# Kernel tuning notes

Hardware: AMD Instinct MI355X
Metric: run time of the kernel (lower is better)

## Reference

```python
import jax, jax.numpy as jnp
import numpy as np

B, N, QD = 2, 4096, 512
HEADS, DIM_HEAD = 8, 64
INNER = HEADS * DIM_HEAD  # 512
SCALE = DIM_HEAD ** -0.5


def setup_inputs() -> dict:
    key = jax.random.key(0)
    ks = jax.random.split(key, 6)
    s = 0.02
    return {
        "x": jax.random.normal(ks[0], (B, N, QD), dtype=jnp.float32),
        "Wq": jax.random.normal(ks[1], (QD, INNER), dtype=jnp.float32) * s,
        "Wk": jax.random.normal(ks[2], (QD, INNER), dtype=jnp.float32) * s,
        "Wv": jax.random.normal(ks[3], (QD, INNER), dtype=jnp.float32) * s,
        "Wo": jax.random.normal(ks[4], (INNER, QD), dtype=jnp.float32) * s,
        "bo": jnp.zeros((QD,), dtype=jnp.float32),
    }


def reference(x, Wq, Wk, Wv, Wo, bo):
    # self-attention: context = x; mask = None; attention_sf = False
    q = x @ Wq  # [B, N, INNER]
    k = x @ Wk
    v = x @ Wv
    # split heads: [B, H, N, D]
    def split(t):
        return t.reshape(B, N, HEADS, DIM_HEAD).transpose(0, 2, 1, 3)
    q, k, v = split(q), split(k), split(v)
    # fp32 QK^T (ATTN_PRECISION='fp32' path)
    sim = jnp.einsum('bhid,bhjd->bhij', q.astype(jnp.float32), k.astype(jnp.float32)) * SCALE
    attn = jax.nn.softmax(sim, axis=-1)
    out = jnp.einsum('bhij,bhjd->bhid', attn, v)  # [B, H, N, D]
    out = out.transpose(0, 2, 1, 3).reshape(B, N, INNER)
    return out @ Wo + bo  # Dropout(p=0) is identity
```

## Files before the change

### kernel.cpp

```cpp
#include <hip/hip_runtime.h>
#include <hip/hip_bf16.h>


typedef __attribute__((ext_vector_type(8))) short short8;
typedef __attribute__((ext_vector_type(4))) float floatx4;
typedef __attribute__((ext_vector_type(16))) float floatx16;

#define MFMA16(a, b, c) __builtin_amdgcn_mfma_f32_16x16x32_bf16((a), (b), (c), 0, 0, 0)
#define MFMA32(a, b, c) __builtin_amdgcn_mfma_f32_32x32x16_bf16((a), (b), (c), 0, 0, 0)

#if __has_builtin(__builtin_amdgcn_exp2f)
#define EXP2(x) __builtin_amdgcn_exp2f(x)
#else
#define EXP2(x) exp2f(x)
#endif

#define QSCALE 0.18033688011112042f

static __device__ __forceinline__ unsigned short f2b(float f) {
  unsigned int u = __float_as_uint(f);
  u += 0x7FFFu + ((u >> 16) & 1u);
  return (unsigned short)(u >> 16);
}

static __device__ __forceinline__ unsigned int pkb(float a, float b) {
  float2 t{a, b};
  __hip_bfloat162 h = __float22bfloat162_rn(t);
  union { __hip_bfloat162 h2; unsigned int u; } cv;
  cv.h2 = h;
  return cv.u;
}

static __device__ __forceinline__ void dma16(const unsigned short* g,
                                             unsigned short* l) {
  __builtin_amdgcn_global_load_lds(
      (const __attribute__((address_space(1))) unsigned int*)g,
      (__attribute__((address_space(3))) unsigned int*)l, 16, 0, 0);
}

__global__ __launch_bounds__(256) void prep_kernel(
    const float* __restrict__ Wq, const float* __restrict__ Wk,
    const float* __restrict__ Wv, const float* __restrict__ Wo,
    const float* __restrict__ x, unsigned short* __restrict__ wtq,
    unsigned short* __restrict__ wtk, unsigned short* __restrict__ wtv,
    unsigned short* __restrict__ wto, unsigned short* __restrict__ xb) {
  const int z = blockIdx.z;
  const int tid = threadIdx.x;
  if (z >= 4) {
    const int bid = (z - 4) * 256 + blockIdx.y * 16 + blockIdx.x;
    const int idx = (bid * 256 + tid) * 8;
    const float4 a = *(const float4*)(x + idx);
    const float4 b = *(const float4*)(x + idx + 4);
    unsigned int u[4] = {pkb(a.x, a.y), pkb(a.z, a.w), pkb(b.x, b.y),
                         pkb(b.z, b.w)};
    *(short8*)(xb + idx) = *(short8*)u;
    return;
  }
  const float* __restrict__ W = (z == 0) ? Wq : (z == 1) ? Wk : (z == 2) ? Wv : Wo;
  unsigned short* __restrict__ T = (z == 0) ? wtq : (z == 1) ? wtk : (z == 2) ? wtv : wto;
  const int k0 = blockIdx.x * 32, c0 = blockIdx.y * 32;
  __shared__ float Ts[32][33];
  const int r = tid >> 3, cc = (tid & 7) * 4;
  const float4 v = *(const float4*)(W + (k0 + r) * 512 + c0 + cc);
  Ts[r][cc] = v.x; Ts[r][cc + 1] = v.y; Ts[r][cc + 2] = v.z; Ts[r][cc + 3] = v.w;
  __syncthreads();
  const unsigned long long uu =
      (unsigned long long)pkb(Ts[cc][r], Ts[cc + 1][r]) |
      ((unsigned long long)pkb(Ts[cc + 2][r], Ts[cc + 3][r]) << 32);
  *(unsigned long long*)(T + (c0 + r) * 512 + k0 + cc) = uu;
}

__global__ __launch_bounds__(256) void qkv_fused_kernel(
    const unsigned short* __restrict__ xb, const unsigned short* __restrict__ wtq,
    const unsigned short* __restrict__ wtk,
    const unsigned short* __restrict__ wtv, unsigned short* __restrict__ qo,
    unsigned short* __restrict__ ko, unsigned short* __restrict__ vo) {
  const int m0 = blockIdx.x * 128;
  const int c0 = blockIdx.y * 32;
  __shared__ __align__(16) unsigned short As[2][128 * 64];
  __shared__ __align__(16) unsigned short Bs[2][3][32 * 64];
  const int tid = threadIdx.x;
  const int lane = tid & 63, w = tid >> 6;
  const int i = lane & 15, q = lane >> 4;
  const int sl = i & 7;
  const int dr = lane >> 3, dc = lane & 7;
  const int sch = (dc ^ dr) * 8;
  const unsigned short* ag = xb + (m0 + w * 32 + dr) * 512 + sch;
  const unsigned short* bg[3];
  bg[0] = wtq + (c0 + w * 8 + dr) * 512 + sch;
  bg[1] = wtk + (c0 + w * 8 + dr) * 512 + sch;
  bg[2] = wtv + (c0 + w * 8 + dr) * 512 + sch;

  floatx4 acc[3][2][2] = {};

#pragma unroll
  for (int p = 0; p < 4; ++p) dma16(ag + p * 8 * 512, &As[0][(w * 32 + p * 8) * 64]);
#pragma unroll
  for (int z = 0; z < 3; ++z) dma16(bg[z], &Bs[0][z][(w * 8) * 64]);
  __syncthreads();

  int buf = 0;
  for (int ks = 0; ks < 8; ++ks) {
    if (ks < 7) {
      const int k1 = (ks + 1) * 64;
#pragma unroll
      for (int p = 0; p < 4; ++p)
        dma16(ag + p * 8 * 512 + k1, &As[buf ^ 1][(w * 32 + p * 8) * 64]);
#pragma unroll
      for (int z = 0; z < 3; ++z)
        dma16(bg[z] + k1, &Bs[buf ^ 1][z][(w * 8) * 64]);
    }
#pragma unroll
    for (int kc = 0; kc < 2; ++kc) {
      short8 af[2];
#pragma unroll
      for (int t = 0; t < 2; ++t)
        af[t] = *(const short8*)&As[buf][(w * 32 + t * 16 + i) * 64 +
                                        (((kc * 4 + q) ^ sl) * 8)];
#pragma unroll
      for (int z = 0; z < 3; ++z)
#pragma unroll
        for (int g = 0; g < 2; ++g) {
          const short8 bf = *(const short8*)&Bs[buf][z][(g * 16 + i) * 64 +
                                                        (((kc * 4 + q) ^ sl) * 8)];
#pragma unroll
          for (int t = 0; t < 2; ++t)
            acc[z][t][g] = MFMA16(af[t], bf, acc[z][t][g]);
        }
    }
    __syncthreads();
    buf ^= 1;
  }
#pragma unroll
  for (int z = 0; z < 3; ++z)
#pragma unroll
    for (int t = 0; t < 2; ++t)
#pragma unroll
      for (int g = 0; g < 2; ++g) {
        const int col = c0 + g * 16 + i;
        const int h = col >> 6, d = col & 63;
        const int row0 = m0 + w * 32 + t * 16 + q * 4;
        const int b = row0 >> 12;
        const int n0 = row0 & 4095;
        if (z == 2) {
          unsigned int* dst =
              (unsigned int*)&vo[(((b * 8 + h) * 64 + d) << 12) + n0];
          dst[0] = pkb(acc[z][t][g][0], acc[z][t][g][1]);
          dst[1] = pkb(acc[z][t][g][2], acc[z][t][g][3]);
        } else {
          unsigned short* dst = (z == 0) ? qo : ko;
          const float sc = (z == 0) ? QSCALE : 1.0f;
#pragma unroll
          for (int r = 0; r < 4; ++r)
            dst[(((b * 8 + h) << 12) + (n0 + r)) * 64 + d] =
                f2b(acc[z][t][g][r] * sc);
        }
      }
}

__global__ __launch_bounds__(512, 4) void flash_kernel(
    const unsigned short* __restrict__ Q, const unsigned short* __restrict__ K,
    const unsigned short* __restrict__ Vt, unsigned short* __restrict__ O) {
  const int bh = blockIdx.x;
  const int m0 = blockIdx.y * 128;
  const int tid = threadIdx.x;
  const int lane = tid & 63, w = tid >> 6;
  const int ql = lane & 31, hi = lane >> 5;
  const int rt = w & 3;
  const int kg = w >> 2;
  const unsigned short* qp = Q + bh * (4096 * 64);
  const unsigned short* kp = K + bh * (4096 * 64);
  const unsigned short* vp = Vt + bh * (64 * 4096);

  __shared__ __align__(16) unsigned short SM[20480];
  unsigned short* Ks = SM + kg * 4096;
  unsigned short* Vs = SM + 8192 + kg * 4096;

  const int srow = (tid & 255) >> 3;
  const int c0s = tid & 7;
  const int sw8 = (c0s ^ (srow & 7)) * 8;
  const unsigned short* kgp = kp + (kg * 2048 + srow) * 64 + c0s * 8;
  const unsigned short* vgp = vp + srow * 4096 + kg * 2048 + c0s * 8;

  short8 qf[4];
  {
    const unsigned short* qrp = qp + (m0 + rt * 32 + ql) * 64 + hi * 8;
#pragma unroll
    for (int ks = 0; ks < 4; ++ks) qf[ks] = *(const short8*)(qrp + ks * 16);
  }

  floatx16 accO[2] = {};
  float accLp = 0.f;
  const int sx = ql & 7;

  *(short8*)&Ks[srow * 64 + sw8] = *(const short8*)(kgp);
  *(short8*)&Ks[(srow + 32) * 64 + sw8] = *(const short8*)(kgp + 32 * 64);
  *(short8*)&Vs[srow * 64 + sw8] = *(const short8*)(vgp);
  *(short8*)&Vs[(srow + 32) * 64 + sw8] = *(const short8*)(vgp + 32 * 4096);
  __syncthreads();

  for (int jt = 0; jt < 32; ++jt) {
    short8 kn0, kn1, vn0, vn1;
    if (jt < 31) {
      kn0 = *(const short8*)(kgp + (jt + 1) * 4096);
      kn1 = *(const short8*)(kgp + (jt + 1) * 4096 + 32 * 64);
      vn0 = *(const short8*)(vgp + (jt + 1) * 64);
      vn1 = *(const short8*)(vgp + (jt + 1) * 64 + 32 * 4096);
    }

    short8 pa[4];
#pragma unroll
    for (int kt = 0; kt < 2; ++kt) {
      floatx16 c;
#pragma unroll
      for (int j = 0; j < 16; ++j) c[j] = 0.0f;
#pragma unroll
      for (int ks = 0; ks < 4; ++ks) {
        const short8 kf = *(const short8*)&Ks[(kt * 32 + ql) * 64 +
                                             (((2 * ks + hi) ^ sx) * 8)];
        c = MFMA32(kf, qf[ks], c);
      }
      float e[16];
#pragma unroll
      for (int j = 0; j < 16; ++j) e[j] = EXP2(c[j]);
      accLp += (((e[0] + e[1]) + (e[2] + e[3])) +
                ((e[4] + e[5]) + (e[6] + e[7]))) +
               (((e[8] + e[9]) + (e[10] + e[11])) +
                ((e[12] + e[13]) + (e[14] + e[15])));
#pragma unroll
      for (int s2 = 0; s2 < 2; ++s2) {
        unsigned int a0 = pkb(e[8 * s2 + 0], e[8 * s2 + 1]);
        unsigned int c1 = pkb(e[8 * s2 + 2], e[8 * s2 + 3]);
        unsigned int b0 = pkb(e[8 * s2 + 4], e[8 * s2 + 5]);
        unsigned int d1 = pkb(e[8 * s2 + 6], e[8 * s2 + 7]);
        asm("v_permlane32_swap_b32 %0, %1" : "+v"(a0), "+v"(b0));
        asm("v_permlane32_swap_b32 %0, %1" : "+v"(c1), "+v"(d1));
        union { unsigned int u[4]; short8 s; } cv;
        cv.u[0] = a0; cv.u[1] = c1; cv.u[2] = b0; cv.u[3] = d1;
        pa[kt * 2 + s2] = cv.s;
      }
    }
#pragma unroll
    for (int dt = 0; dt < 2; ++dt)
#pragma unroll
      for (int ks2 = 0; ks2 < 4; ++ks2) {
        const short8 vf = *(const short8*)&Vs[(dt * 32 + ql) * 64 +
                                              (((2 * ks2 + hi) ^ sx) * 8)];
        accO[dt] = MFMA32(pa[ks2], vf, accO[dt]);
      }
    __syncthreads();
    if (jt < 31) {
      *(short8*)&Ks[srow * 64 + sw8] = kn0;
      *(short8*)&Ks[(srow + 32) * 64 + sw8] = kn1;
      *(short8*)&Vs[srow * 64 + sw8] = vn0;
      *(short8*)&Vs[(srow + 32) * 64 + sw8] = vn1;
    }
    __syncthreads();
  }

  float* MB = (float*)SM;
  if (kg == 1) {
    float* dst = MB + (rt * 64 + lane) * 40;
#pragma unroll
    for (int dt = 0; dt < 2; ++dt)
#pragma unroll
      for (int r = 0; r < 16; ++r) dst[dt * 16 + r] = accO[dt][r];
    dst[32] = accLp;
  }
  __syncthreads();
  if (kg == 1) return;
  {
    const float* src = MB + (rt * 64 + lane) * 40;
#pragma unroll
    for (int dt = 0; dt < 2; ++dt)
#pragma unroll
      for (int r = 0; r < 16; ++r) accO[dt][r] += src[dt * 16 + r];
    accLp += src[32];
  }

  const float Lfull = accLp + __shfl(accLp, lane ^ 32, 64);
  const float invL = 1.0f / Lfull;
  const int b = bh >> 3, h = bh & 7;
#pragma unroll
  for (int r = 0; r < 16; ++r) {
    const int qrow = (r & 3) + 8 * (r >> 2) + 4 * hi;
    const float iv = __shfl(invL, qrow, 64);
    const int n = m0 + rt * 32 + qrow;
#pragma unroll
    for (int dt = 0; dt < 2; ++dt) {
      const int col = h * 64 + dt * 32 + ql;
      O[((b << 12) + n) * 512 + col] = f2b(accO[dt][r] * iv);
    }
  }
}

__global__ __launch_bounds__(256) void out_proj_kernel(
    const unsigned short* __restrict__ A, const unsigned short* __restrict__ wto,
    const float* __restrict__ bo, float* __restrict__ out) {
  const int m0 = blockIdx.x * 64, c0 = blockIdx.y * 64;
  __shared__ __align__(16) unsigned short As[2][64 * 64];
  __shared__ __align__(16) unsigned short Bs[2][64 * 64];
  const int tid = threadIdx.x;
  const int lane = tid & 63, w = tid >> 6;
  const int i = lane & 15, q = lane >> 4;
  const int wy = w >> 1, wx = w & 1;
  const int sl = i & 7;
  const int dr = lane >> 3, dc = lane & 7;
  const int sch = (dc ^ dr) * 8;
  const unsigned short* ag = A + (m0 + w * 16 + dr) * 512 + sch;
  const unsigned short* bg = wto + (c0 + w * 16 + dr) * 512 + sch;

  floatx4 acc[2][2] = {};
#pragma unroll
  for (int p = 0; p < 2; ++p) {
    dma16(ag + p * 8 * 512, &As[0][(w * 16 + p * 8) * 64]);
    dma16(bg + p * 8 * 512, &Bs[0][(w * 16 + p * 8) * 64]);
  }
  __syncthreads();

  int buf = 0;
  for (int ks = 0; ks < 8; ++ks) {
    if (ks < 7) {
      const int k1 = (ks + 1) * 64;
#pragma unroll
      for (int p = 0; p < 2; ++p) {
        dma16(ag + p * 8 * 512 + k1, &As[buf ^ 1][(w * 16 + p * 8) * 64]);
        dma16(bg + p * 8 * 512 + k1, &Bs[buf ^ 1][(w * 16 + p * 8) * 64]);
      }
    }
#pragma unroll
    for (int kc = 0; kc < 2; ++kc) {
      short8 af[2], bfr[2];
#pragma unroll
      for (int t = 0; t < 2; ++t)
        af[t] = *(const short8*)&As[buf][(wy * 32 + t * 16 + i) * 64 +
                                        (((kc * 4 + q) ^ sl) * 8)];
#pragma unroll
      for (int g = 0; g < 2; ++g)
        bfr[g] = *(const short8*)&Bs[buf][(wx * 32 + g * 16 + i) * 64 +
                                          (((kc * 4 + q) ^ sl) * 8)];
#pragma unroll
      for (int t = 0; t < 2; ++t)
#pragma unroll
        for (int g = 0; g < 2; ++g) acc[t][g] = MFMA16(af[t], bfr[g], acc[t][g]);
    }
    __syncthreads();
    buf ^= 1;
  }
#pragma unroll
  for (int t = 0; t < 2; ++t)
#pragma unroll
    for (int g = 0; g < 2; ++g) {
      const int col = c0 + wx * 32 + g * 16 + i;
      const float bias = bo[col];
#pragma unroll
      for (int r = 0; r < 4; ++r) {
        const int row = m0 + wy * 32 + t * 16 + q * 4 + r;
        out[row * 512 + col] = acc[t][g][r] + bias;
      }
    }
}

extern "C" void kernel_launch(void* const* d_in, const int* in_sizes, int n_in,
                              void* d_out, int out_size, void* d_ws,
                              size_t ws_size, hipStream_t stream) {
  const float* x = (const float*)d_in[0];
  const float* Wq = (const float*)d_in[1];
  const float* Wk = (const float*)d_in[2];
  const float* Wv = (const float*)d_in[3];
  const float* Wo = (const float*)d_in[4];
  const float* bo = (const float*)d_in[5];
  float* out = (float*)d_out;

  const size_t tsz = (size_t)16 * 4096 * 64;
  unsigned short* qws = (unsigned short*)d_ws;
  unsigned short* kws = qws + tsz;
  unsigned short* vws = kws + tsz;
  unsigned short* ows = vws + tsz;
  unsigned short* wtq = ows + tsz;
  unsigned short* wtk = wtq + 512 * 512;
  unsigned short* wtv = wtk + 512 * 512;
  unsigned short* wto = wtv + 512 * 512;
  unsigned short* xb = wto + 512 * 512;

  prep_kernel<<<dim3(16, 16, 12), 256, 0, stream>>>(Wq, Wk, Wv, Wo, x, wtq,
                                                    wtk, wtv, wto, xb);
  qkv_fused_kernel<<<dim3(64, 16), 256, 0, stream>>>(xb, wtq, wtk, wtv, qws,
                                                     kws, vws);
  flash_kernel<<<dim3(16, 32), 512, 0, stream>>>(qws, kws, vws, ows);
  out_proj_kernel<<<dim3(128, 8), 256, 0, stream>>>(ows, wto, bo, out);
}
```

Measured before the change: 195.9 us.

## Double-buffer K/V shared tiles and raise wave priority around MFMA blocks

Shared memory grows to hold two K/V tile buffers per key group. The next tile is written into the alternate buffer right after compute, so one of the two __syncthreads per iteration can be dropped. s_setprio hints are also placed around the QK and PV MFMA loops to favour matrix issue. The larger LDS footprint (64KB per block) may reduce how many blocks fit per CU against the launch bound of 4.

Result: no change. 194.2 us, median of 2 (-0.9%).

```diff
diff --git a/kernel.cpp b/kernel.cpp
--- a/kernel.cpp
+++ b/kernel.cpp
@@ -172,9 +172,9 @@
   const unsigned short* kp = K + bh * (4096 * 64);
   const unsigned short* vp = Vt + bh * (64 * 4096);
 
-  __shared__ __align__(16) unsigned short SM[20480];
-  unsigned short* Ks = SM + kg * 4096;
-  unsigned short* Vs = SM + 8192 + kg * 4096;
+  __shared__ __align__(16) unsigned short SM[32768];
+  unsigned short* Ksb = SM + kg * 4096;
+  unsigned short* Vsb = SM + 16384 + kg * 4096;
 
   const int srow = (tid & 255) >> 3;
   const int c0s = tid & 7;
@@ -193,12 +193,13 @@
   float accLp = 0.f;
   const int sx = ql & 7;
 
-  *(short8*)&Ks[srow * 64 + sw8] = *(const short8*)(kgp);
-  *(short8*)&Ks[(srow + 32) * 64 + sw8] = *(const short8*)(kgp + 32 * 64);
-  *(short8*)&Vs[srow * 64 + sw8] = *(const short8*)(vgp);
-  *(short8*)&Vs[(srow + 32) * 64 + sw8] = *(const short8*)(vgp + 32 * 4096);
+  *(short8*)&Ksb[srow * 64 + sw8] = *(const short8*)(kgp);
+  *(short8*)&Ksb[(srow + 32) * 64 + sw8] = *(const short8*)(kgp + 32 * 64);
+  *(short8*)&Vsb[srow * 64 + sw8] = *(const short8*)(vgp);
+  *(short8*)&Vsb[(srow + 32) * 64 + sw8] = *(const short8*)(vgp + 32 * 4096);
   __syncthreads();
 
+  int buf = 0;
   for (int jt = 0; jt < 32; ++jt) {
     short8 kn0, kn1, vn0, vn1;
     if (jt < 31) {
@@ -207,6 +208,8 @@
       vn0 = *(const short8*)(vgp + (jt + 1) * 64);
       vn1 = *(const short8*)(vgp + (jt + 1) * 64 + 32 * 4096);
     }
+    const unsigned short* Ks = Ksb + buf * 8192;
+    const unsigned short* Vs = Vsb + buf * 8192;
 
     short8 pa[4];
 #pragma unroll
@@ -214,12 +217,14 @@
       floatx16 c;
 #pragma unroll
       for (int j = 0; j < 16; ++j) c[j] = 0.0f;
+      __builtin_amdgcn_s_setprio(1);
 #pragma unroll
       for (int ks = 0; ks < 4; ++ks) {
         const short8 kf = *(const short8*)&Ks[(kt * 32 + ql) * 64 +
                                              (((2 * ks + hi) ^ sx) * 8)];
         c = MFMA32(kf, qf[ks], c);
       }
+      __builtin_amdgcn_s_setprio(0);
       float e[16];
 #pragma unroll
       for (int j = 0; j < 16; ++j) e[j] = EXP2(c[j]);
@@ -240,6 +245,7 @@
         pa[kt * 2 + s2] = cv.s;
       }
     }
+    __builtin_amdgcn_s_setprio(1);
 #pragma unroll
     for (int dt = 0; dt < 2; ++dt)
 #pragma unroll
@@ -248,14 +254,17 @@
                                               (((2 * ks2 + hi) ^ sx) * 8)];
         accO[dt] = MFMA32(pa[ks2], vf, accO[dt]);
       }
+    __builtin_amdgcn_s_setprio(0);
+    if (jt < 31) {
+      unsigned short* Kw = Ksb + (buf ^ 1) * 8192;
+      unsigned short* Vw = Vsb + (buf ^ 1) * 8192;
+      *(short8*)&Kw[srow * 64 + sw8] = kn0;
+      *(short8*)&Kw[(srow + 32) * 64 + sw8] = kn1;
+      *(short8*)&Vw[srow * 64 + sw8] = vn0;
+      *(short8*)&Vw[(srow + 32) * 64 + sw8] = vn1;
+    }
     __syncthreads();
-    if (jt < 31) {
-      *(short8*)&Ks[srow * 64 + sw8] = kn0;
-      *(short8*)&Ks[(srow + 32) * 64 + sw8] = kn1;
-      *(short8*)&Vs[srow * 64 + sw8] = vn0;
-      *(short8*)&Vs[(srow + 32) * 64 + sw8] = vn1;
-    }
-    __syncthreads();
+    buf ^= 1;
   }
 
   float* MB = (float*)SM;
```
